# Optimization experiments

Hardware: AMD Instinct MI355X
Metric: run time of the kernel (lower is better)

The kernel has to match this reference:

```python
import jax, jax.numpy as jnp
import numpy as np

N = 50000
E = 800000
NEG_SLOPE = 0.2
LN_EPS = 1e-5


def _layer_norm(x, g, b):
    mu = jnp.mean(x, axis=-1, keepdims=True)
    var = jnp.mean(jnp.square(x - mu), axis=-1, keepdims=True)
    return (x - mu) * jax.lax.rsqrt(var + LN_EPS) * g + b


def _gat(x, src, dst, W, a_s, a_d, bias, concat):
    # x: [N, Fin], W: [Fin, H*C], a_s/a_d: [H, C]
    H, C = a_s.shape
    h = (x @ W).reshape(N, H, C)
    # per-node attention logits (PyG GATConv style)
    als = jnp.sum(h * a_s, axis=-1)  # [N, H] from source nodes
    ald = jnp.sum(h * a_d, axis=-1)  # [N, H] from target nodes
    e = jax.nn.leaky_relu(als[src] + ald[dst], negative_slope=NEG_SLOPE)  # [E', H]
    # segment softmax over incoming edges of each target node
    m = jax.ops.segment_max(e, dst, num_segments=N)
    m = jnp.where(jnp.isfinite(m), m, 0.0)  # guard empty segments
    ex = jnp.exp(e - m[dst])
    denom = jax.ops.segment_sum(ex, dst, num_segments=N)
    alpha = ex / (denom[dst] + 1e-16)  # [E', H]
    out = jax.ops.segment_sum(h[src] * alpha[:, :, None], dst, num_segments=N)  # [N, H, C]
    out = out.reshape(N, H * C) if concat else jnp.mean(out, axis=1)
    return out + bias


def setup_inputs() -> dict:
    key = jax.random.key(0)
    ks = jax.random.split(key, 20)
    H, C = 4, 64
    d_in, d_hid, d_out = 128, H * C, 64
    g = lambda k, shape, fan: jax.random.normal(k, shape, jnp.float32) * (1.0 / np.sqrt(fan))
    return {
        "x": jax.random.normal(ks[0], (N, d_in), jnp.float32),
        "edge_index": jax.random.randint(ks[1], (2, E), 0, N, jnp.int64),
        "W1": g(ks[2], (d_in, H * C), d_in), "a1s": g(ks[3], (H, C), C), "a1d": g(ks[4], (H, C), C),
        "b1": jnp.zeros((d_hid,), jnp.float32), "ln1_g": jnp.ones((d_hid,), jnp.float32), "ln1_b": jnp.zeros((d_hid,), jnp.float32),
        "W2": g(ks[5], (d_hid, H * C), d_hid), "a2s": g(ks[6], (H, C), C), "a2d": g(ks[7], (H, C), C),
        "b2": jnp.zeros((d_hid,), jnp.float32), "ln2_g": jnp.ones((d_hid,), jnp.float32), "ln2_b": jnp.zeros((d_hid,), jnp.float32),
        "W3": g(ks[8], (d_hid, 1 * d_out), d_hid), "a3s": g(ks[9], (1, d_out), d_out), "a3d": g(ks[10], (1, d_out), d_out),
        "b3": jnp.zeros((d_out,), jnp.float32),
    }


def reference(x, edge_index, W1, a1s, a1d, b1, ln1_g, ln1_b,
              W2, a2s, a2d, b2, ln2_g, ln2_b, W3, a3s, a3d, b3):
    # add self loops (GATConv default add_self_loops=True)
    loops = jnp.arange(N, dtype=edge_index.dtype)
    src = jnp.concatenate([edge_index[0], loops])
    dst = jnp.concatenate([edge_index[1], loops])
    h = _gat(x, src, dst, W1, a1s, a1d, b1, concat=True)
    h = jax.nn.relu(_layer_norm(h, ln1_g, ln1_b))  # dropout = identity (eval)
    h = _gat(h, src, dst, W2, a2s, a2d, b2, concat=True)
    h = jax.nn.relu(_layer_norm(h, ln2_g, ln2_b))
    out = _gat(h, src, dst, W3, a3s, a3d, b3, concat=False)
    return out
```

## Files before the change

### kernel.cpp

```cpp
#include <hip/hip_runtime.h>
#include <math.h>


typedef _Float16 half8 __attribute__((ext_vector_type(8)));
typedef _Float16 half4v __attribute__((ext_vector_type(4)));
typedef _Float16 half2v __attribute__((ext_vector_type(2)));
typedef float float4v __attribute__((ext_vector_type(4)));

#define CSRW 64

__device__ inline float leaky02(float v) { return (v > 0.f) ? v : 0.2f * v; }

__device__ inline void gload_lds16(const void* g, void* l) {
  __builtin_amdgcn_global_load_lds(
      (const __attribute__((address_space(1))) unsigned int*)g,
      (__attribute__((address_space(3))) unsigned int*)l, 16, 0, 0);
}

__global__ void k_scatter_prep(const int* __restrict__ ei, int E, int N,
                               int* __restrict__ cnt, int* __restrict__ colidx,
                               const float* __restrict__ x,
                               _Float16* __restrict__ xh,
                               const float* __restrict__ W1,
                               _Float16* __restrict__ Wt1,
                               const float* __restrict__ W2,
                               _Float16* __restrict__ Wt2,
                               const float* __restrict__ W3,
                               _Float16* __restrict__ Wt3, int n4) {
  int t = blockIdx.x * blockDim.x + threadIdx.x;
  int ET = E + N;
  if (t < ET) {
    int s, d;
    if (t < E) { s = ei[t]; d = ei[E + t]; } else { s = t - E; d = t - E; }
    int pos = atomicAdd(&cnt[d], 1);
    if (pos < CSRW) colidx[d * CSRW + pos] = s;
    return;
  }
  t -= ET;
  if (t < n4) {
    float4 v = ((const float4*)x)[t];
    half4v h = {(_Float16)v.x, (_Float16)v.y, (_Float16)v.z, (_Float16)v.w};
    ((half4v*)xh)[t] = h;
    return;
  }
  t -= n4;
  if (t < 128 * 256) {
    int n = t >> 7, k = t & 127;
    Wt1[t] = (_Float16)W1[(size_t)k * 256 + n];
    return;
  }
  t -= 128 * 256;
  if (t < 256 * 256) {
    int n = t >> 8, k = t & 255;
    Wt2[t] = (_Float16)W2[(size_t)k * 256 + n];
    return;
  }
  t -= 256 * 256;
  if (t < 256 * 64) {
    int n = t >> 8, k = t & 255;
    Wt3[t] = (_Float16)W3[(size_t)k * 64 + n];
  }
}

template <int BN, int TM, int TN, int WGN, int H>
__global__ __launch_bounds__(256) void k_gemm_mfma(
    const _Float16* __restrict__ A, const _Float16* __restrict__ Bt,
    _Float16* __restrict__ C, const float* __restrict__ a_s,
    const float* __restrict__ a_d, float* __restrict__ als,
    float* __restrict__ ald, int M, int K, int Nc) {
  __shared__ _Float16 As[128 * 64];
  __shared__ _Float16 Bs[BN * 64];
  int tid = threadIdx.x;
  int row0 = blockIdx.y * 128, col0 = blockIdx.x * BN;
  int w = tid >> 6, lane = tid & 63;
  int quad = lane >> 4, lr = lane & 15;
  int wm0 = (w / WGN) * (TM * 16);
  int wn0 = (w % WGN) * (TN * 16);
  float4v acc[TM][TN] = {};
  for (int k0 = 0; k0 < K; k0 += 64) {
#pragma unroll
    for (int t = 0; t < 4; t++) {
      int G = (w * 4 + t) * 64 + lane;
      int r = G >> 3, c = G & 7;
      int cg = c ^ (r & 7);
      if (row0 + r < M)
        gload_lds16(A + (size_t)(row0 + r) * K + k0 + cg * 8,
                    As + (w * 4 + t) * 512);
    }
#pragma unroll
    for (int t = 0; t < BN / 32; t++) {
      int G = (w * (BN / 32) + t) * 64 + lane;
      int n = G >> 3, c = G & 7;
      int cg = c ^ (n & 7);
      gload_lds16(Bt + (size_t)(col0 + n) * K + k0 + cg * 8,
                  Bs + (w * (BN / 32) + t) * 512);
    }
    __syncthreads();
#pragma unroll
    for (int kk = 0; kk < 2; kk++) {
      half8 af[TM], bf[TN];
#pragma unroll
      for (int i = 0; i < TM; i++) {
        int rl = wm0 + i * 16 + lr;
        int p = kk * 4 + quad;
        af[i] = *(half8*)&As[rl * 64 + ((p ^ (rl & 7)) * 8)];
      }
#pragma unroll
      for (int j = 0; j < TN; j++) {
        int nl = wn0 + j * 16 + lr;
        int p = kk * 4 + quad;
        bf[j] = *(half8*)&Bs[nl * 64 + ((p ^ (nl & 7)) * 8)];
      }
#pragma unroll
      for (int i = 0; i < TM; i++)
#pragma unroll
        for (int j = 0; j < TN; j++)
          acc[i][j] = __builtin_amdgcn_mfma_f32_16x16x32_f16(bf[j], af[i],
                                                             acc[i][j], 0, 0, 0);
    }
    __syncthreads();
  }
#pragma unroll
  for (int i = 0; i < TM; i++) {
    int row = row0 + wm0 + i * 16 + lr;
    if (row < M) {
#pragma unroll
      for (int j = 0; j < TN; j++) {
        half4v o = {(_Float16)acc[i][j][0], (_Float16)acc[i][j][1],
                    (_Float16)acc[i][j][2], (_Float16)acc[i][j][3]};
        *(half4v*)(C + (size_t)row * Nc + col0 + wn0 + j * 16 + quad * 4) = o;
      }
    }
  }
  int hd = (col0 + wn0) >> 6;
  float4 as4[TN], ad4[TN];
#pragma unroll
  for (int j = 0; j < TN; j++) {
    as4[j] = *(const float4*)(a_s + hd * 64 + j * 16 + quad * 4);
    ad4[j] = *(const float4*)(a_d + hd * 64 + j * 16 + quad * 4);
  }
#pragma unroll
  for (int i = 0; i < TM; i++) {
    float ps = 0.f, pd = 0.f;
#pragma unroll
    for (int j = 0; j < TN; j++) {
      ps += acc[i][j][0] * as4[j].x + acc[i][j][1] * as4[j].y +
            acc[i][j][2] * as4[j].z + acc[i][j][3] * as4[j].w;
      pd += acc[i][j][0] * ad4[j].x + acc[i][j][1] * ad4[j].y +
            acc[i][j][2] * ad4[j].z + acc[i][j][3] * ad4[j].w;
    }
    ps += __shfl_xor(ps, 16, 64);
    ps += __shfl_xor(ps, 32, 64);
    pd += __shfl_xor(pd, 16, 64);
    pd += __shfl_xor(pd, 32, 64);
    int row = row0 + wm0 + i * 16 + lr;
    if (quad == 0 && row < M) {
      als[(size_t)row * H + hd] = ps;
      ald[(size_t)row * H + hd] = pd;
    }
  }
}

__global__ void k_gather4(const _Float16* __restrict__ h,
                          const float* __restrict__ als,
                          const float* __restrict__ ald,
                          const int* __restrict__ cnt,
                          const int* __restrict__ colidx,
                          const float* __restrict__ bias,
                          const float* __restrict__ ln_g,
                          const float* __restrict__ ln_b,
                          _Float16* __restrict__ out, int N) {
  int wid = (blockIdx.x * blockDim.x + threadIdx.x) >> 6;
  int lane = threadIdx.x & 63;
  int half = lane >> 5, l = lane & 31;
  int node = wid * 2 + half;
  bool active = node < N;
  int hd = l >> 3;
  int ch = l * 8;
  float aldh = active ? ald[(size_t)node * 4 + hd] : 0.f;
  half2v acc[4] = {};
  float wsum = 0.f;
  int e0 = node * CSRW;
  int e1 = active ? e0 + min(cnt[node], CSRW) : e0;
  int e = e0;
  for (; e + 4 <= e1; e += 4) {
    int s0 = colidx[e], s1 = colidx[e + 1], s2 = colidx[e + 2],
        s3 = colidx[e + 3];
    float v0 = als[(size_t)s0 * 4 + hd], v1 = als[(size_t)s1 * 4 + hd],
          v2 = als[(size_t)s2 * 4 + hd], v3 = als[(size_t)s3 * 4 + hd];
    uint4 r0 = *(const uint4*)(h + (size_t)s0 * 256 + ch);
    uint4 r1 = *(const uint4*)(h + (size_t)s1 * 256 + ch);
    uint4 r2 = *(const uint4*)(h + (size_t)s2 * 256 + ch);
    uint4 r3 = *(const uint4*)(h + (size_t)s3 * 256 + ch);
    float w0 = __expf(fminf(leaky02(v0 + aldh), 19.f) - 8.f);
    float w1 = __expf(fminf(leaky02(v1 + aldh), 19.f) - 8.f);
    float w2 = __expf(fminf(leaky02(v2 + aldh), 19.f) - 8.f);
    float w3 = __expf(fminf(leaky02(v3 + aldh), 19.f) - 8.f);
    wsum += (w0 + w1) + (w2 + w3);
    _Float16 h0 = (_Float16)w0, h1 = (_Float16)w1, h2 = (_Float16)w2,
             h3 = (_Float16)w3;
    half2v W0 = {h0, h0}, W1 = {h1, h1}, W2 = {h2, h2}, W3 = {h3, h3};
    acc[0] += W0 * __builtin_bit_cast(half2v, r0.x) +
              W1 * __builtin_bit_cast(half2v, r1.x) +
              W2 * __builtin_bit_cast(half2v, r2.x) +
              W3 * __builtin_bit_cast(half2v, r3.x);
    acc[1] += W0 * __builtin_bit_cast(half2v, r0.y) +
              W1 * __builtin_bit_cast(half2v, r1.y) +
              W2 * __builtin_bit_cast(half2v, r2.y) +
              W3 * __builtin_bit_cast(half2v, r3.y);
    acc[2] += W0 * __builtin_bit_cast(half2v, r0.z) +
              W1 * __builtin_bit_cast(half2v, r1.z) +
              W2 * __builtin_bit_cast(half2v, r2.z) +
              W3 * __builtin_bit_cast(half2v, r3.z);
    acc[3] += W0 * __builtin_bit_cast(half2v, r0.w) +
              W1 * __builtin_bit_cast(half2v, r1.w) +
              W2 * __builtin_bit_cast(half2v, r2.w) +
              W3 * __builtin_bit_cast(half2v, r3.w);
  }
  for (; e < e1; e++) {
    int s = colidx[e];
    float v = als[(size_t)s * 4 + hd];
    uint4 r = *(const uint4*)(h + (size_t)s * 256 + ch);
    float w = __expf(fminf(leaky02(v + aldh), 19.f) - 8.f);
    wsum += w;
    _Float16 hw = (_Float16)w;
    half2v W = {hw, hw};
    acc[0] += W * __builtin_bit_cast(half2v, r.x);
    acc[1] += W * __builtin_bit_cast(half2v, r.y);
    acc[2] += W * __builtin_bit_cast(half2v, r.z);
    acc[3] += W * __builtin_bit_cast(half2v, r.w);
  }
  float invl = active ? (1.f / wsum) : 0.f;
  float4 bA = active ? *(const float4*)(bias + ch) : float4{0, 0, 0, 0};
  float4 bB = active ? *(const float4*)(bias + ch + 4) : float4{0, 0, 0, 0};
  float y[8];
  y[0] = (float)acc[0].x * invl + bA.x;
  y[1] = (float)acc[0].y * invl + bA.y;
  y[2] = (float)acc[1].x * invl + bA.z;
  y[3] = (float)acc[1].y * invl + bA.w;
  y[4] = (float)acc[2].x * invl + bB.x;
  y[5] = (float)acc[2].y * invl + bB.y;
  y[6] = (float)acc[3].x * invl + bB.z;
  y[7] = (float)acc[3].y * invl + bB.w;
  float s1 = 0.f;
#pragma unroll
  for (int k = 0; k < 8; k++) s1 += y[k];
#pragma unroll
  for (int msk = 16; msk > 0; msk >>= 1) s1 += __shfl_xor(s1, msk, 64);
  float mu = s1 * (1.0f / 256.0f);
  float s2 = 0.f;
#pragma unroll
  for (int k = 0; k < 8; k++) {
    float d = y[k] - mu;
    s2 += d * d;
  }
#pragma unroll
  for (int msk = 16; msk > 0; msk >>= 1) s2 += __shfl_xor(s2, msk, 64);
  float rstd = rsqrtf(s2 * (1.0f / 256.0f) + 1e-5f);
  if (active) {
    float4 gA = *(const float4*)(ln_g + ch), gB = *(const float4*)(ln_g + ch + 4);
    float4 eA = *(const float4*)(ln_b + ch), eB = *(const float4*)(ln_b + ch + 4);
    half8 o;
    o[0] = (_Float16)fmaxf((y[0] - mu) * rstd * gA.x + eA.x, 0.f);
    o[1] = (_Float16)fmaxf((y[1] - mu) * rstd * gA.y + eA.y, 0.f);
    o[2] = (_Float16)fmaxf((y[2] - mu) * rstd * gA.z + eA.z, 0.f);
    o[3] = (_Float16)fmaxf((y[3] - mu) * rstd * gA.w + eA.w, 0.f);
    o[4] = (_Float16)fmaxf((y[4] - mu) * rstd * gB.x + eB.x, 0.f);
    o[5] = (_Float16)fmaxf((y[5] - mu) * rstd * gB.y + eB.y, 0.f);
    o[6] = (_Float16)fmaxf((y[6] - mu) * rstd * gB.z + eB.z, 0.f);
    o[7] = (_Float16)fmaxf((y[7] - mu) * rstd * gB.w + eB.w, 0.f);
    *(half8*)(out + (size_t)node * 256 + ch) = o;
  }
}

__global__ void k_gather1(const _Float16* __restrict__ h,
                          const float* __restrict__ als,
                          const float* __restrict__ ald,
                          const int* __restrict__ cnt,
                          const int* __restrict__ colidx,
                          const float* __restrict__ bias,
                          float* __restrict__ out, int N) {
  int node = (blockIdx.x * blockDim.x + threadIdx.x) >> 6;
  int lane = threadIdx.x & 63;
  if (node >= N) return;
  int g = lane >> 3, t = lane & 7, ch = t * 8;
  float aldn = ald[node];
  float acc[8] = {};
  float wsum = 0.f;
  int e0 = node * CSRW;
  int e1 = e0 + min(cnt[node], CSRW);
  int e = e0 + g;
  for (; e + 8 < e1; e += 16) {
    int sA = colidx[e], sB = colidx[e + 8];
    float vA = als[sA], vB = als[sB];
    uint4 rA = *(const uint4*)(h + (size_t)sA * 64 + ch);
    uint4 rB = *(const uint4*)(h + (size_t)sB * 64 + ch);
    float wA = __expf(fminf(leaky02(vA + aldn), 19.f) - 8.f);
    float wB = __expf(fminf(leaky02(vB + aldn), 19.f) - 8.f);
    wsum += wA + wB;
    const half2v* pA = (const half2v*)&rA;
    const half2v* pB = (const half2v*)&rB;
#pragma unroll
    for (int k = 0; k < 4; k++) {
      half2v a2 = pA[k], b2 = pB[k];
      acc[2 * k + 0] += wA * (float)a2.x + wB * (float)b2.x;
      acc[2 * k + 1] += wA * (float)a2.y + wB * (float)b2.y;
    }
  }
  if (e < e1) {
    int s = colidx[e];
    float v = als[s];
    uint4 r = *(const uint4*)(h + (size_t)s * 64 + ch);
    float w = __expf(fminf(leaky02(v + aldn), 19.f) - 8.f);
    wsum += w;
    const half2v* p = (const half2v*)&r;
#pragma unroll
    for (int k = 0; k < 4; k++) {
      half2v a2 = p[k];
      acc[2 * k + 0] += w * (float)a2.x;
      acc[2 * k + 1] += w * (float)a2.y;
    }
  }
#pragma unroll
  for (int msk = 8; msk <= 32; msk <<= 1) {
#pragma unroll
    for (int k = 0; k < 8; k++) acc[k] += __shfl_xor(acc[k], msk, 64);
    wsum += __shfl_xor(wsum, msk, 64);
  }
  if (g == 0) {
    float invl = 1.f / wsum;
    float4 bA = *(const float4*)(bias + ch), bB = *(const float4*)(bias + ch + 4);
    float4 o0 = make_float4(acc[0] * invl + bA.x, acc[1] * invl + bA.y,
                            acc[2] * invl + bA.z, acc[3] * invl + bA.w);
    float4 o1 = make_float4(acc[4] * invl + bB.x, acc[5] * invl + bB.y,
                            acc[6] * invl + bB.z, acc[7] * invl + bB.w);
    *(float4*)(out + (size_t)node * 64 + ch) = o0;
    *(float4*)(out + (size_t)node * 64 + ch + 4) = o1;
  }
}

extern "C" void kernel_launch(void* const* d_in, const int* in_sizes, int n_in,
                              void* d_out, int out_size, void* d_ws,
                              size_t ws_size, hipStream_t stream) {
  const float* x   = (const float*)d_in[0];
  const int*   ei  = (const int*)d_in[1];
  const float* W1  = (const float*)d_in[2];
  const float* a1s = (const float*)d_in[3];
  const float* a1d = (const float*)d_in[4];
  const float* b1  = (const float*)d_in[5];
  const float* g1  = (const float*)d_in[6];
  const float* be1 = (const float*)d_in[7];
  const float* W2  = (const float*)d_in[8];
  const float* a2s = (const float*)d_in[9];
  const float* a2d = (const float*)d_in[10];
  const float* b2  = (const float*)d_in[11];
  const float* g2  = (const float*)d_in[12];
  const float* be2 = (const float*)d_in[13];
  const float* W3  = (const float*)d_in[14];
  const float* a3s = (const float*)d_in[15];
  const float* a3d = (const float*)d_in[16];
  const float* b3  = (const float*)d_in[17];
  float* out = (float*)d_out;

  const int Nn = in_sizes[0] / 128;
  const int E  = in_sizes[1] / 2;
  const int ET = E + Nn;

  char* wsb = (char*)d_ws;
  size_t off = 0;
  auto alloc = [&](size_t bytes) -> void* {
    void* p = wsb + off;
    off += (bytes + 255) & ~(size_t)255;
    return p;
  };
  _Float16* xh   = (_Float16*)alloc((size_t)Nn * 256 * 2);
  _Float16* hbuf = (_Float16*)alloc((size_t)Nn * 256 * 2);
  _Float16* Wt1  = (_Float16*)alloc(128 * 256 * 2);
  _Float16* Wt2  = (_Float16*)alloc(256 * 256 * 2);
  _Float16* Wt3  = (_Float16*)alloc(256 * 64 * 2);
  float* als  = (float*)alloc((size_t)Nn * 4 * 4);
  float* ald  = (float*)alloc((size_t)Nn * 4 * 4);
  int* cnt    = (int*)alloc((size_t)Nn * 4);
  int* colidx = (int*)alloc((size_t)Nn * CSRW * 4);
  (void)ws_size;

  hipMemsetAsync(cnt, 0, (size_t)Nn * 4, stream);
  int n4 = Nn * 128 / 4;
  int total = ET + n4 + 128 * 256 + 256 * 256 + 256 * 64;
  k_scatter_prep<<<(total + 255) / 256, 256, 0, stream>>>(
      ei, E, Nn, cnt, colidx, x, xh, W1, Wt1, W2, Wt2, W3, Wt3, n4);

  int nwb4 = (Nn + 7) / 8;
  int nwb1 = (Nn + 3) / 4;
  dim3 g128(2, (Nn + 127) / 128);
  dim3 g64(1, (Nn + 127) / 128);

  k_gemm_mfma<128, 4, 4, 2, 4><<<g128, 256, 0, stream>>>(
      xh, Wt1, hbuf, a1s, a1d, als, ald, Nn, 128, 256);
  k_gather4<<<nwb4, 256, 0, stream>>>(hbuf, als, ald, cnt, colidx, b1, g1, be1,
                                      xh, Nn);
  k_gemm_mfma<128, 4, 4, 2, 4><<<g128, 256, 0, stream>>>(
      xh, Wt2, hbuf, a2s, a2d, als, ald, Nn, 256, 256);
  k_gather4<<<nwb4, 256, 0, stream>>>(hbuf, als, ald, cnt, colidx, b2, g2, be2,
                                      xh, Nn);
  k_gemm_mfma<64, 2, 4, 1, 1><<<g64, 256, 0, stream>>>(
      xh, Wt3, hbuf, a3s, a3d, als, ald, Nn, 256, 64);
  k_gather1<<<nwb1, 256, 0, stream>>>(hbuf, als, ald, cnt, colidx, b3, out, Nn);
}
```

Measured before the change: 370.4 us.

## Fuse layer-1 GEMM with fp32 input conversion and CSR scatter in one launch

Layer 1's GEMM now reads fp32 x directly, converts it to fp16 in LDS and computes the full K=128 in a single tile. It runs in the same grid as the edge-scatter and W2/W3 transpose blocks, with W1 transposed in its own small kernel beforehand. This removes the separate x-to-fp16 pass and a GEMM launch, and lets the atomic scatter overlap with the MFMA work. The CSR column indices shrink to 16-bit, halving index traffic in the gathers. This relies on node ids fitting in 16 bits, but N=50000 fits. The GEMM block also uses large LDS (about 67KB), which may limit occupancy.

```diff
diff --git a/kernel.cpp b/kernel.cpp
--- a/kernel.cpp
+++ b/kernel.cpp
@@ -17,48 +17,163 @@
       (__attribute__((address_space(3))) unsigned int*)l, 16, 0, 0);
 }
 
-__global__ void k_scatter_prep(const int* __restrict__ ei, int E, int N,
-                               int* __restrict__ cnt, int* __restrict__ colidx,
-                               const float* __restrict__ x,
-                               _Float16* __restrict__ xh,
-                               const float* __restrict__ W1,
-                               _Float16* __restrict__ Wt1,
-                               const float* __restrict__ W2,
-                               _Float16* __restrict__ Wt2,
-                               const float* __restrict__ W3,
-                               _Float16* __restrict__ Wt3, int n4) {
+__global__ void k_wt1(const float* __restrict__ W1, _Float16* __restrict__ Wt1) {
   int t = blockIdx.x * blockDim.x + threadIdx.x;
-  int ET = E + N;
-  if (t < ET) {
-    int s, d;
-    if (t < E) { s = ei[t]; d = ei[E + t]; } else { s = t - E; d = t - E; }
-    int pos = atomicAdd(&cnt[d], 1);
-    if (pos < CSRW) colidx[d * CSRW + pos] = s;
-    return;
-  }
-  t -= ET;
-  if (t < n4) {
-    float4 v = ((const float4*)x)[t];
-    half4v h = {(_Float16)v.x, (_Float16)v.y, (_Float16)v.z, (_Float16)v.w};
-    ((half4v*)xh)[t] = h;
-    return;
-  }
-  t -= n4;
   if (t < 128 * 256) {
     int n = t >> 7, k = t & 127;
     Wt1[t] = (_Float16)W1[(size_t)k * 256 + n];
+  }
+}
+
+__global__ __launch_bounds__(256) void k_fused1(
+    const float* __restrict__ x, const _Float16* __restrict__ Wt1,
+    _Float16* __restrict__ hbuf, const float* __restrict__ a_s,
+    const float* __restrict__ a_d, float* __restrict__ als,
+    float* __restrict__ ald, const int* __restrict__ ei, int E, int N,
+    int* __restrict__ cnt, unsigned short* __restrict__ colidx,
+    const float* __restrict__ W2, _Float16* __restrict__ Wt2,
+    const float* __restrict__ W3, _Float16* __restrict__ Wt3, int ng1,
+    int nsc) {
+  __shared__ _Float16 As[128 * 132];
+  __shared__ _Float16 Bs[128 * 132];
+  int b = blockIdx.x;
+  if (b < ng1) {
+    const int M = N;
+    int bx = b & 1, by = b >> 1;
+    int row0 = by * 128, col0 = bx * 128;
+    int tid = threadIdx.x;
+    int w = tid >> 6, lane = tid & 63;
+    int quad = lane >> 4, lr = lane & 15;
+    int wm0 = (w >> 1) * 64;
+    int wn0 = (w & 1) * 64;
+    {
+      int r = tid >> 1, hf = tid & 1;
+      int gr = row0 + r;
+      _Float16* dst = As + r * 132 + hf * 64;
+      if (gr < M) {
+        const float4* src = (const float4*)(x + (size_t)gr * 128 + hf * 64);
+#pragma unroll
+        for (int c = 0; c < 8; c++) {
+          float4 v0 = src[2 * c], v1 = src[2 * c + 1];
+          half8 hv = {(_Float16)v0.x, (_Float16)v0.y, (_Float16)v0.z,
+                      (_Float16)v0.w, (_Float16)v1.x, (_Float16)v1.y,
+                      (_Float16)v1.z, (_Float16)v1.w};
+          *(half8*)(dst + c * 8) = hv;
+        }
+      } else {
+#pragma unroll
+        for (int c = 0; c < 8; c++) *(half8*)(dst + c * 8) = half8{};
+      }
+    }
+    {
+      int n = tid >> 1, hf = tid & 1;
+      const half8* src = (const half8*)(Wt1 + (size_t)(col0 + n) * 128 + hf * 64);
+      _Float16* dst = Bs + n * 132 + hf * 64;
+#pragma unroll
+      for (int c = 0; c < 8; c++) *(half8*)(dst + c * 8) = src[c];
+    }
+    __syncthreads();
+    float4v acc[4][4] = {};
+#pragma unroll
+    for (int kk = 0; kk < 4; kk++) {
+      half8 af[4], bf[4];
+#pragma unroll
+      for (int i = 0; i < 4; i++)
+        af[i] = *(half8*)&As[(wm0 + i * 16 + lr) * 132 + kk * 32 + quad * 8];
+#pragma unroll
+      for (int j = 0; j < 4; j++)
+        bf[j] = *(half8*)&Bs[(wn0 + j * 16 + lr) * 132 + kk * 32 + quad * 8];
+#pragma unroll
+      for (int i = 0; i < 4; i++)
+#pragma unroll
+        for (int j = 0; j < 4; j++)
+          acc[i][j] = __builtin_amdgcn_mfma_f32_16x16x32_f16(bf[j], af[i],
+                                                             acc[i][j], 0, 0, 0);
+    }
+#pragma unroll
+    for (int i = 0; i < 4; i++) {
+      int row = row0 + wm0 + i * 16 + lr;
+      if (row < M) {
+#pragma unroll
+        for (int j = 0; j < 4; j++) {
+          half4v o = {(_Float16)acc[i][j][0], (_Float16)acc[i][j][1],
+                      (_Float16)acc[i][j][2], (_Float16)acc[i][j][3]};
+          *(half4v*)(hbuf + (size_t)row * 256 + col0 + wn0 + j * 16 + quad * 4) = o;
+        }
+      }
+    }
+    int hd = (col0 + wn0) >> 6;
+    float4 as4[4], ad4[4];
+#pragma unroll
+    for (int j = 0; j < 4; j++) {
+      as4[j] = *(const float4*)(a_s + hd * 64 + j * 16 + quad * 4);
+      ad4[j] = *(const float4*)(a_d + hd * 64 + j * 16 + quad * 4);
+    }
+#pragma unroll
+    for (int i = 0; i < 4; i++) {
+      float ps = 0.f, pd = 0.f;
+#pragma unroll
+      for (int j = 0; j < 4; j++) {
+        ps += acc[i][j][0] * as4[j].x + acc[i][j][1] * as4[j].y +
+              acc[i][j][2] * as4[j].z + acc[i][j][3] * as4[j].w;
+        pd += acc[i][j][0] * ad4[j].x + acc[i][j][1] * ad4[j].y +
+              acc[i][j][2] * ad4[j].z + acc[i][j][3] * ad4[j].w;
+      }
+      ps += __shfl_xor(ps, 16, 64);
+      ps += __shfl_xor(ps, 32, 64);
+      pd += __shfl_xor(pd, 16, 64);
+      pd += __shfl_xor(pd, 32, 64);
+      int row = row0 + wm0 + i * 16 + lr;
+      if (quad == 0 && row < M) {
+        als[(size_t)row * 4 + hd] = ps;
+        ald[(size_t)row * 4 + hd] = pd;
+      }
+    }
     return;
   }
-  t -= 128 * 256;
-  if (t < 256 * 256) {
-    int n = t >> 8, k = t & 255;
-    Wt2[t] = (_Float16)W2[(size_t)k * 256 + n];
+  b -= ng1;
+  if (b < nsc) {
+    int ET = E + N;
+    int b4 = (b * 256 + threadIdx.x) * 4;
+    if (b4 >= ET) return;
+    if (b4 + 3 < E) {
+      int4 s4 = *(const int4*)(ei + b4);
+      int4 d4 = *(const int4*)(ei + E + b4);
+      int p0 = atomicAdd(&cnt[d4.x], 1);
+      int p1 = atomicAdd(&cnt[d4.y], 1);
+      int p2 = atomicAdd(&cnt[d4.z], 1);
+      int p3 = atomicAdd(&cnt[d4.w], 1);
+      if (p0 < CSRW) colidx[d4.x * CSRW + p0] = (unsigned short)s4.x;
+      if (p1 < CSRW) colidx[d4.y * CSRW + p1] = (unsigned short)s4.y;
+      if (p2 < CSRW) colidx[d4.z * CSRW + p2] = (unsigned short)s4.z;
+      if (p3 < CSRW) colidx[d4.w * CSRW + p3] = (unsigned short)s4.w;
+    } else {
+#pragma unroll
+      for (int q = 0; q < 4; q++) {
+        int e = b4 + q;
+        if (e < ET) {
+          int s, d;
+          if (e < E) { s = ei[e]; d = ei[E + e]; } else { s = e - E; d = e - E; }
+          int pos = atomicAdd(&cnt[d], 1);
+          if (pos < CSRW) colidx[d * CSRW + pos] = (unsigned short)s;
+        }
+      }
+    }
     return;
   }
-  t -= 256 * 256;
-  if (t < 256 * 64) {
-    int n = t >> 8, k = t & 255;
-    Wt3[t] = (_Float16)W3[(size_t)k * 64 + n];
+  b -= nsc;
+  {
+    int t = b * 256 + threadIdx.x;
+    if (t < 256 * 256) {
+      int n = t >> 8, k = t & 255;
+      Wt2[t] = (_Float16)W2[(size_t)k * 256 + n];
+      return;
+    }
+    t -= 256 * 256;
+    if (t < 256 * 64) {
+      int n = t >> 8, k = t & 255;
+      Wt3[t] = (_Float16)W3[(size_t)k * 64 + n];
+    }
   }
 }
 
@@ -165,7 +280,7 @@
                           const float* __restrict__ als,
                           const float* __restrict__ ald,
                           const int* __restrict__ cnt,
-                          const int* __restrict__ colidx,
+                          const unsigned short* __restrict__ colidx,
                           const float* __restrict__ bias,
                           const float* __restrict__ ln_g,
                           const float* __restrict__ ln_b,
@@ -277,7 +392,7 @@
                           const float* __restrict__ als,
                           const float* __restrict__ ald,
                           const int* __restrict__ cnt,
-                          const int* __restrict__ colidx,
+                          const unsigned short* __restrict__ colidx,
                           const float* __restrict__ bias,
                           float* __restrict__ out, int N) {
   int node = (blockIdx.x * blockDim.x + threadIdx.x) >> 6;
@@ -373,37 +488,39 @@
     off += (bytes + 255) & ~(size_t)255;
     return p;
   };
-  _Float16* xh   = (_Float16*)alloc((size_t)Nn * 256 * 2);
+  _Float16* ah   = (_Float16*)alloc((size_t)Nn * 256 * 2);
   _Float16* hbuf = (_Float16*)alloc((size_t)Nn * 256 * 2);
   _Float16* Wt1  = (_Float16*)alloc(128 * 256 * 2);
   _Float16* Wt2  = (_Float16*)alloc(256 * 256 * 2);
   _Float16* Wt3  = (_Float16*)alloc(256 * 64 * 2);
-  float* als  = (float*)alloc((size_t)Nn * 4 * 4);
-  float* ald  = (float*)alloc((size_t)Nn * 4 * 4);
-  int* cnt    = (int*)alloc((size_t)Nn * 4);
-  int* colidx = (int*)alloc((size_t)Nn * CSRW * 4);
+  float* als = (float*)alloc((size_t)Nn * 4 * 4);
+  float* ald = (float*)alloc((size_t)Nn * 4 * 4);
+  int* cnt   = (int*)alloc((size_t)Nn * 4);
+  unsigned short* colidx = (unsigned short*)alloc((size_t)Nn * CSRW * 2);
   (void)ws_size;
 
   hipMemsetAsync(cnt, 0, (size_t)Nn * 4, stream);
-  int n4 = Nn * 128 / 4;
-  int total = ET + n4 + 128 * 256 + 256 * 256 + 256 * 64;
-  k_scatter_prep<<<(total + 255) / 256, 256, 0, stream>>>(
-      ei, E, Nn, cnt, colidx, x, xh, W1, Wt1, W2, Wt2, W3, Wt3, n4);
+  k_wt1<<<(128 * 256 + 255) / 256, 256, 0, stream>>>(W1, Wt1);
+
+  int ng1 = 2 * ((Nn + 127) / 128);
+  int nsc = ((ET + 3) / 4 + 255) / 256;
+  int ntr = (256 * 256 + 256 * 64 + 255) / 256;
+  k_fused1<<<ng1 + nsc + ntr, 256, 0, stream>>>(
+      x, Wt1, hbuf, a1s, a1d, als, ald, ei, E, Nn, cnt, colidx, W2, Wt2, W3,
+      Wt3, ng1, nsc);
 
   int nwb4 = (Nn + 7) / 8;
   int nwb1 = (Nn + 3) / 4;
   dim3 g128(2, (Nn + 127) / 128);
   dim3 g64(1, (Nn + 127) / 128);
 
+  k_gather4<<<nwb4, 256, 0, stream>>>(hbuf, als, ald, cnt, colidx, b1, g1, be1,
+                                      ah, Nn);
   k_gemm_mfma<128, 4, 4, 2, 4><<<g128, 256, 0, stream>>>(
-      xh, Wt1, hbuf, a1s, a1d, als, ald, Nn, 128, 256);
-  k_gather4<<<nwb4, 256, 0, stream>>>(hbuf, als, ald, cnt, colidx, b1, g1, be1,
-                                      xh, Nn);
-  k_gemm_mfma<128, 4, 4, 2, 4><<<g128, 256, 0, stream>>>(
-      xh, Wt2, hbuf, a2s, a2d, als, ald, Nn, 256, 256);
+      ah, Wt2, hbuf, a2s, a2d, als, ald, Nn, 256, 256);
   k_gather4<<<nwb4, 256, 0, stream>>>(hbuf, als, ald, cnt, colidx, b2, g2, be2,
-                                      xh, Nn);
+                                      ah, Nn);
   k_gemm_mfma<64, 2, 4, 1, 1><<<g64, 256, 0, stream>>>(
-      xh, Wt3, hbuf, a3s, a3d, als, ald, Nn, 256, 64);
+      ah, Wt3, hbuf, a3s, a3d, als, ald, Nn, 256, 64);
   k_gather1<<<nwb1, 256, 0, stream>>>(hbuf, als, ald, cnt, colidx, b3, out, Nn);
 }
```

Measured after the change: 368.0 us. Within noise of the previous version (-0.7%).
